# Kernel tuning notes

Measured on AMD Instinct MI355X. Metric: run time of the kernel, lower is better.

## Reference

```python
import jax, jax.numpy as jnp
import numpy as np
from jax import lax

EPS = 1e-3  # keras BatchNormalization default epsilon

def _bn(x, g, b, m, v):
    # inference-mode batchnorm over channel axis (last)
    return (x - m) * (g * lax.rsqrt(v + EPS)) + b

def _cond_dw(h, Wdw, bdw, rw):
    # h: [B,H,W,M]; Wdw: [E,3,3,M]; bdw: [E,M]; rw: [B,E]
    E, M = Wdw.shape[0], Wdw.shape[-1]
    out = jnp.zeros_like(h)
    for i in range(E):  # small fixed expert count
        k = Wdw[i].reshape(3, 3, 1, M)  # depthwise kernel, groups=M
        y = lax.conv_general_dilated(
            h, k, window_strides=(1, 1), padding='SAME',
            dimension_numbers=('NHWC', 'HWIO', 'NHWC'),
            feature_group_count=M) + bdw[i]
        out = out + y * rw[:, i, None, None, None]
    return out

def setup_inputs() -> dict:
    key = jax.random.key(0)
    ks = jax.random.split(key, 24)
    B, H, W, C = 32, 56, 56, 96
    E, M, F = 4, 384, 96
    d = {}
    d['x'] = jax.random.normal(ks[0], (B, H, W, C), jnp.float32)
    d['Wr'] = jax.random.normal(ks[1], (C, E), jnp.float32) * 0.1
    d['br'] = jax.random.normal(ks[2], (E,), jnp.float32) * 0.1
    d['Wpw'] = jax.random.normal(ks[3], (E, C, M), jnp.float32) * (2.0 / C) ** 0.5
    d['bpw'] = jax.random.normal(ks[4], (E, M), jnp.float32) * 0.01
    d['Wdw'] = jax.random.normal(ks[5], (E, 3, 3, M), jnp.float32) * 0.1
    d['bdw'] = jax.random.normal(ks[6], (E, M), jnp.float32) * 0.01
    d['Wpwl'] = jax.random.normal(ks[7], (E, M, F), jnp.float32) * (2.0 / M) ** 0.5
    d['bpwl'] = jax.random.normal(ks[8], (E, F), jnp.float32) * 0.01
    d['g1'] = jax.random.uniform(ks[9], (M,), jnp.float32, 0.5, 1.5)
    d['b1'] = jax.random.normal(ks[10], (M,), jnp.float32) * 0.1
    d['m1'] = jax.random.normal(ks[11], (M,), jnp.float32) * 0.1
    d['v1'] = jax.random.uniform(ks[12], (M,), jnp.float32, 0.5, 1.5)
    d['g2'] = jax.random.uniform(ks[13], (M,), jnp.float32, 0.5, 1.5)
    d['b2'] = jax.random.normal(ks[14], (M,), jnp.float32) * 0.1
    d['m2'] = jax.random.normal(ks[15], (M,), jnp.float32) * 0.1
    d['v2'] = jax.random.uniform(ks[16], (M,), jnp.float32, 0.5, 1.5)
    d['g3'] = jax.random.uniform(ks[17], (F,), jnp.float32, 0.5, 1.5)
    d['b3'] = jax.random.normal(ks[18], (F,), jnp.float32) * 0.1
    d['m3'] = jax.random.normal(ks[19], (F,), jnp.float32) * 0.1
    d['v3'] = jax.random.uniform(ks[20], (F,), jnp.float32, 0.5, 1.5)
    return d

def reference(x, Wr, br, Wpw, bpw, Wdw, bdw, Wpwl, bpwl,
              g1, b1, m1, v1, g2, b2, m2, v2, g3, b3, m3, v3):
    shortcut = x
    # routing: global avg pool + dense + sigmoid
    pooled = jnp.mean(x, axis=(1, 2))                      # [B,C]
    rw = jax.nn.sigmoid(pooled @ Wr + br)                  # [B,E]
    # cond pointwise expand: combine 1x1 expert kernels per-sample (linear in kernel)
    Wk = jnp.einsum('be,ecm->bcm', rw, Wpw)
    h = jnp.einsum('bhwc,bcm->bhwm', x, Wk) + (rw @ bpw)[:, None, None, :]
    h = jax.nn.relu(_bn(h, g1, b1, m1, v1))
    # cond depthwise 3x3
    h = _cond_dw(h, Wdw, bdw, rw)
    h = jax.nn.relu(_bn(h, g2, b2, m2, v2))
    # cond pointwise project
    Wk2 = jnp.einsum('be,emf->bmf', rw, Wpwl)
    h = jnp.einsum('bhwm,bmf->bhwf', h, Wk2) + (rw @ bpwl)[:, None, None, :]
    h = _bn(h, g3, b3, m3, v3)
    return h + shortcut
```

## Files before the change

### kernel.cpp

```cpp
#include <hip/hip_runtime.h>

#define B_ 32
#define HH 56
#define WW 56
#define C_ 96
#define E_ 4
#define M_ 384
#define F_ 96
#define P_ 3136
#define EPS 1e-3f

typedef __attribute__((ext_vector_type(8))) __bf16 bf16x8;
typedef __attribute__((ext_vector_type(8))) short short8;
typedef __attribute__((ext_vector_type(4))) float f32x4;
typedef __attribute__((ext_vector_type(2))) float f32x2;
typedef __attribute__((ext_vector_type(4))) unsigned short us4;
typedef unsigned short u16;

__device__ __forceinline__ float bf2f(u16 s) {
  union { unsigned u; float f; } c;
  c.u = ((unsigned)s) << 16;
  return c.f;
}
__device__ __forceinline__ u16 f2bf(float f) {
  union { float f; unsigned u; } c;
  c.f = f;
  unsigned u = c.u + 0x7FFFu + ((c.u >> 16) & 1u);
  return (u16)(u >> 16);
}
__device__ __forceinline__ f32x2 bfpair(unsigned u) {
  union { unsigned i; float f; } lo, hi;
  lo.i = u << 16;
  hi.i = u & 0xffff0000u;
  f32x2 r;
  r.x = lo.f;
  r.y = hi.f;
  return r;
}

__global__ __launch_bounds__(256) void k_pool(
    const float* __restrict__ x, float* __restrict__ partial) {
  int chunk = blockIdx.x, b = blockIdx.y;
  int p0 = chunk * 49;
  const float* xb = x + ((size_t)b * P_ + p0) * C_;
  int t = threadIdx.x;
  int c4 = t % 24, s = t / 24;
  __shared__ f32x4 part[10][24];
  if (s < 10) {
    f32x4 sum = {0.f, 0.f, 0.f, 0.f};
    for (int p = s; p < 49; p += 10)
      sum += *(const f32x4*)&xb[(size_t)p * C_ + c4 * 4];
    part[s][c4] = sum;
  }
  __syncthreads();
  if (s == 0) {
    f32x4 acc = part[0][c4];
#pragma unroll
    for (int ss = 1; ss < 10; ++ss) acc += part[ss][c4];
    *(f32x4*)&partial[(((size_t)b * 64 + chunk)) * C_ + c4 * 4] = acc;
  }
}

__global__ __launch_bounds__(128) void k_routing2(
    const float* __restrict__ partial, const float* __restrict__ Wr,
    const float* __restrict__ br, float* __restrict__ rw) {
  int b = blockIdx.x;
  int c = threadIdx.x;
  __shared__ float pooled[C_];
  if (c < C_) {
    float s = 0.f;
    for (int ch = 0; ch < 64; ++ch) s += partial[((size_t)b * 64 + ch) * C_ + c];
    pooled[c] = s * (1.f / (float)P_);
  }
  __syncthreads();
  if (c < E_) {
    float acc = br[c];
    for (int cc = 0; cc < C_; ++cc) acc += pooled[cc] * Wr[cc * E_ + c];
    rw[b * E_ + c] = 1.f / (1.f + expf(-acc));
  }
}

__global__ __launch_bounds__(256) void k_mkall(
    const float* __restrict__ Wpw, const float* __restrict__ bpw,
    const float* __restrict__ Wdw, const float* __restrict__ bdw,
    const float* __restrict__ Wpwl, const float* __restrict__ bpwl,
    const float* __restrict__ rw,
    const float* __restrict__ g1, const float* __restrict__ b1,
    const float* __restrict__ m1, const float* __restrict__ v1,
    const float* __restrict__ g2, const float* __restrict__ b2,
    const float* __restrict__ m2, const float* __restrict__ v2,
    const float* __restrict__ g3, const float* __restrict__ b3,
    const float* __restrict__ m3, const float* __restrict__ v3,
    u16* __restrict__ Wk_t, float* __restrict__ bias1p,
    float* __restrict__ Wdwf_t,
    u16* __restrict__ Wk2_t, float* __restrict__ bias3p) {
  int b = blockIdx.x, seg = blockIdx.y;
  float r0 = rw[b * 4 + 0], r1 = rw[b * 4 + 1], r2 = rw[b * 4 + 2], r3 = rw[b * 4 + 3];
  int t = threadIdx.x;
  if (seg < 6) {
    __shared__ __align__(16) u16 tile[64][104];
    int ml = t & 63;
    int m = seg * 64 + ml, cp = t >> 6;
    float s1 = g1[m] * rsqrtf(v1[m] + EPS);
#pragma unroll
    for (int j = 0; j < 24; ++j) {
      int c = cp + 4 * j;
      float w = r0 * Wpw[(0 * C_ + c) * M_ + m] + r1 * Wpw[(1 * C_ + c) * M_ + m] +
                r2 * Wpw[(2 * C_ + c) * M_ + m] + r3 * Wpw[(3 * C_ + c) * M_ + m];
      tile[ml][c] = f2bf(w * s1);
    }
    __syncthreads();
    u16* dst = Wk_t + ((size_t)b * M_ + seg * 64) * C_;
#pragma unroll
    for (int k = 0; k < 3; ++k) {
      int ch = t + 256 * k;
      int mr = ch / 12, off = (ch % 12) * 8;
      *(short8*)&dst[(size_t)mr * C_ + off] = *(const short8*)&tile[mr][off];
    }
  } else if (seg == 6) {
    for (int m = t; m < M_; m += 256) {
      float s2 = g2[m] * rsqrtf(v2[m] + EPS);
      int oct = m >> 3, q = m & 7;
      float* base = Wdwf_t + ((size_t)b * 48 + oct) * 80;
#pragma unroll
      for (int tap = 0; tap < 9; ++tap) {
        float w = r0 * Wdw[(0 * 9 + tap) * M_ + m] + r1 * Wdw[(1 * 9 + tap) * M_ + m] +
                  r2 * Wdw[(2 * 9 + tap) * M_ + m] + r3 * Wdw[(3 * 9 + tap) * M_ + m];
        base[tap * 8 + q] = w * s2;
      }
      float bias = r0 * bdw[m] + r1 * bdw[M_ + m] + r2 * bdw[2 * M_ + m] + r3 * bdw[3 * M_ + m];
      base[72 + q] = (bias - m2[m]) * s2 + b2[m];
      float s1 = g1[m] * rsqrtf(v1[m] + EPS);
      float bb = r0 * bpw[m] + r1 * bpw[M_ + m] + r2 * bpw[2 * M_ + m] + r3 * bpw[3 * M_ + m];
      bias1p[b * M_ + m] = (bb - m1[m]) * s1 + b1[m];
    }
    if (t < F_) {
      float s3 = g3[t] * rsqrtf(v3[t] + EPS);
      float bb = r0 * bpwl[t] + r1 * bpwl[F_ + t] + r2 * bpwl[2 * F_ + t] + r3 * bpwl[3 * F_ + t];
      bias3p[b * F_ + t] = (bb - m3[t]) * s3 + b3[t];
    }
  } else {
    __shared__ __align__(16) u16 tile2[96][72];
    int m0 = (seg - 7) * 64;
#pragma unroll
    for (int j = 0; j < 24; ++j) {
      int id = t + 256 * j;
      int m = id / 96, f = id % 96;
      float w = r0 * Wpwl[(0 * M_ + m0 + m) * F_ + f] + r1 * Wpwl[(1 * M_ + m0 + m) * F_ + f] +
                r2 * Wpwl[(2 * M_ + m0 + m) * F_ + f] + r3 * Wpwl[(3 * M_ + m0 + m) * F_ + f];
      float s3 = g3[f] * rsqrtf(v3[f] + EPS);
      tile2[f][m] = f2bf(w * s3);
    }
    __syncthreads();
    u16* dst = Wk2_t + (size_t)b * F_ * M_ + m0;
#pragma unroll
    for (int k = 0; k < 3; ++k) {
      int ch = t + 256 * k;
      int f = ch / 8, off = (ch % 8) * 8;
      *(short8*)&dst[(size_t)f * M_ + off] = *(const short8*)&tile2[f][off];
    }
  }
}

__global__ __launch_bounds__(256) void k_expand(
    const float* __restrict__ x, const u16* __restrict__ Wk_t,
    const float* __restrict__ bias1p, u16* __restrict__ h1) {
  __shared__ __align__(16) u16 As[64][104];
  __shared__ __align__(16) u16 Bs[64][104];
  int pt = blockIdx.x, b = blockIdx.y;
  int p0 = pt * 64;
  int t = threadIdx.x;
  const float* A = x + ((size_t)b * P_ + p0) * C_;
#pragma unroll
  for (int j = 0; j < 6; ++j) {
    int ch = t + 256 * j;
    int r = ch / 24, o = (ch % 24) * 4;
    f32x4 v = *(const f32x4*)&A[(size_t)r * C_ + o];
    unsigned lo_, hi_;
    asm("v_cvt_pk_bf16_f32 %0, %1, %2" : "=v"(lo_) : "v"(v.x), "v"(v.y));
    asm("v_cvt_pk_bf16_f32 %0, %1, %2" : "=v"(hi_) : "v"(v.z), "v"(v.w));
    uint2 st = {lo_, hi_};
    *(uint2*)&As[r][o] = st;
  }
  const u16* Bt = Wk_t + (size_t)b * M_ * C_;
  u16* out = h1 + (size_t)b * P_ * M_;
  int lane = t & 63, w = t >> 6;
  int rA = w * 16 + (lane & 15);
  int k0 = (lane >> 4) * 8;
  __syncthreads();
  for (int nt = 0; nt < 6; ++nt) {
    if (nt) __syncthreads();
#pragma unroll
    for (int j = 0; j < 3; ++j) {
      int ch = t + 256 * j;
      int r = ch / 12, o = (ch % 12) * 8;
      *(short8*)&Bs[r][o] = *(const short8*)&Bt[((size_t)(nt * 64 + r)) * C_ + o];
    }
    __syncthreads();
    f32x4 acc[4] = {};
#pragma unroll
    for (int kc = 0; kc < 3; ++kc) {
      bf16x8 a = *(const bf16x8*)&As[rA][kc * 32 + k0];
#pragma unroll
      for (int ct = 0; ct < 4; ++ct) {
        bf16x8 bb = *(const bf16x8*)&Bs[ct * 16 + (lane & 15)][kc * 32 + k0];
        acc[ct] = __builtin_amdgcn_mfma_f32_16x16x32_bf16(a, bb, acc[ct], 0, 0, 0);
      }
    }
    int rowb = p0 + w * 16 + (lane >> 4) * 4;
    int n0 = nt * 64;
#pragma unroll
    for (int ct = 0; ct < 4; ++ct) {
      int m = n0 + ct * 16 + (lane & 15);
      float bias = bias1p[b * M_ + m];
#pragma unroll
      for (int i = 0; i < 4; ++i) {
        float v = fmaxf(acc[ct][i] + bias, 0.f);
        out[(size_t)(rowb + i) * M_ + m] = f2bf(v);
      }
    }
  }
}

struct Row { f32x2 v[3][4]; };
__global__ __launch_bounds__(128) void k_dw(
    const u16* __restrict__ h1, const float* __restrict__ Wdwf_t,
    u16* __restrict__ h2) {
  int b = blockIdx.z;
  int t = blockIdx.x * 128 + threadIdx.x;
  int xw = t / 48, oct = t % 48;
  int y0 = blockIdx.y * 7;
  const float* wo = Wdwf_t + ((size_t)b * 48 + oct) * 80;
  f32x2 w2[40];
#pragma unroll
  for (int i = 0; i < 40; ++i) w2[i] = *(const f32x2*)&wo[i * 2];
  const u16* inp = h1 + (size_t)b * P_ * M_ + oct * 8;
  u16* outp = h2 + (size_t)b * P_ * M_ + oct * 8;

  auto loadr = [&](Row& r, int yy) {
    bool rowok = ((unsigned)yy < 56u);
#pragma unroll
    for (int dx = 0; dx < 3; ++dx) {
      int xx = xw + dx - 1;
      uint4 u = {0u, 0u, 0u, 0u};
      if (rowok && ((unsigned)xx < 56u))
        u = *(const uint4*)&inp[((size_t)yy * 56 + xx) * M_];
      r.v[dx][0] = bfpair(u.x);
      r.v[dx][1] = bfpair(u.y);
      r.v[dx][2] = bfpair(u.z);
      r.v[dx][3] = bfpair(u.w);
    }
  };
  auto comp = [&](int y, const Row& A, const Row& B, const Row& C) {
    f32x2 acc[4];
#pragma unroll
    for (int j = 0; j < 4; ++j) acc[j] = w2[36 + j];
#pragma unroll
    for (int dx = 0; dx < 3; ++dx) {
#pragma unroll
      for (int j = 0; j < 4; ++j) {
        acc[j] += A.v[dx][j] * w2[(0 + dx) * 4 + j];
        acc[j] += B.v[dx][j] * w2[(3 + dx) * 4 + j];
        acc[j] += C.v[dx][j] * w2[(6 + dx) * 4 + j];
      }
    }
    unsigned o[4];
#pragma unroll
    for (int j = 0; j < 4; ++j) {
      float lo = fmaxf(acc[j].x, 0.f), hi = fmaxf(acc[j].y, 0.f);
      asm("v_cvt_pk_bf16_f32 %0, %1, %2" : "=v"(o[j]) : "v"(lo), "v"(hi));
    }
    uint4 st = {o[0], o[1], o[2], o[3]};
    *(uint4*)&outp[((size_t)y * 56 + xw) * M_] = st;
  };

  Row ra, rb, rc, rd;
  loadr(ra, y0 - 1);
  loadr(rb, y0);
  loadr(rc, y0 + 1);
  loadr(rd, y0 + 2);
  comp(y0 + 0, ra, rb, rc);
  loadr(ra, y0 + 3);
  comp(y0 + 1, rb, rc, rd);
  loadr(rb, y0 + 4);
  comp(y0 + 2, rc, rd, ra);
  loadr(rc, y0 + 5);
  comp(y0 + 3, rd, ra, rb);
  loadr(rd, y0 + 6);
  comp(y0 + 4, ra, rb, rc);
  loadr(ra, y0 + 7);
  comp(y0 + 5, rb, rc, rd);
  comp(y0 + 6, rc, rd, ra);
}

__global__ __launch_bounds__(256) void k_proj(
    const u16* __restrict__ h2, const u16* __restrict__ Wk2_t,
    const float* __restrict__ bias3p, const float* __restrict__ xres,
    float* __restrict__ outp) {
  __shared__ __align__(16) u16 As[64][104];
  __shared__ __align__(16) u16 Bs[96][104];
  int b = blockIdx.z, pt = blockIdx.x;
  int p0 = pt * 64;
  int t = threadIdx.x;
  const u16* A = h2 + ((size_t)b * P_ + p0) * M_;
  const u16* Bt = Wk2_t + (size_t)b * F_ * M_;
  int lane = t & 63, w = t >> 6;
  int rA = w * 16 + (lane & 15);
  int k0 = (lane >> 4) * 8;
  f32x4 acc[6] = {};
  for (int kc = 0; kc < 4; ++kc) {
    if (kc) __syncthreads();
#pragma unroll
    for (int j = 0; j < 3; ++j) {
      int ch = t + 256 * j;
      int r = ch / 12, o = (ch % 12) * 8;
      *(short8*)&As[r][o] = *(const short8*)&A[(size_t)r * M_ + kc * 96 + o];
    }
#pragma unroll
    for (int j = 0; j < 5; ++j) {
      int ch = t + 256 * j;
      if (ch < 96 * 12) {
        int r = ch / 12, o = (ch % 12) * 8;
        *(short8*)&Bs[r][o] = *(const short8*)&Bt[(size_t)r * M_ + kc * 96 + o];
      }
    }
    __syncthreads();
#pragma unroll
    for (int ks = 0; ks < 3; ++ks) {
      bf16x8 a = *(const bf16x8*)&As[rA][ks * 32 + k0];
#pragma unroll
      for (int ct = 0; ct < 6; ++ct) {
        bf16x8 bb = *(const bf16x8*)&Bs[ct * 16 + (lane & 15)][ks * 32 + k0];
        acc[ct] = __builtin_amdgcn_mfma_f32_16x16x32_bf16(a, bb, acc[ct], 0, 0, 0);
      }
    }
  }
  const float* xr = xres + (size_t)b * P_ * F_;
  float* op = outp + (size_t)b * P_ * F_;
  int rowb = p0 + w * 16 + (lane >> 4) * 4;
#pragma unroll
  for (int ct = 0; ct < 6; ++ct) {
    int f = ct * 16 + (lane & 15);
    float bias = bias3p[b * F_ + f];
#pragma unroll
    for (int i = 0; i < 4; ++i) {
      size_t idx = (size_t)(rowb + i) * F_ + f;
      op[idx] = acc[ct][i] + bias + xr[idx];
    }
  }
}

extern "C" void kernel_launch(void* const* d_in, const int* in_sizes, int n_in,
                              void* d_out, int out_size, void* d_ws, size_t ws_size,
                              hipStream_t stream) {
  (void)in_sizes; (void)n_in; (void)out_size; (void)ws_size;
  const float* x    = (const float*)d_in[0];
  const float* Wr   = (const float*)d_in[1];
  const float* br   = (const float*)d_in[2];
  const float* Wpw  = (const float*)d_in[3];
  const float* bpw  = (const float*)d_in[4];
  const float* Wdw  = (const float*)d_in[5];
  const float* bdw  = (const float*)d_in[6];
  const float* Wpwl = (const float*)d_in[7];
  const float* bpwl = (const float*)d_in[8];
  const float* g1 = (const float*)d_in[9];
  const float* b1 = (const float*)d_in[10];
  const float* m1 = (const float*)d_in[11];
  const float* v1 = (const float*)d_in[12];
  const float* g2 = (const float*)d_in[13];
  const float* b2 = (const float*)d_in[14];
  const float* m2 = (const float*)d_in[15];
  const float* v2 = (const float*)d_in[16];
  const float* g3 = (const float*)d_in[17];
  const float* b3 = (const float*)d_in[18];
  const float* m3 = (const float*)d_in[19];
  const float* v3 = (const float*)d_in[20];
  float* out = (float*)d_out;

  char* p = (char*)d_ws;
  auto alloc = [&](size_t bytes) {
    char* r = p;
    p += (bytes + 255) & ~(size_t)255;
    return r;
  };
  float* rw      = (float*)alloc((size_t)B_ * E_ * 4);
  float* partial = (float*)alloc((size_t)B_ * 64 * C_ * 4);
  u16*   Wk_t    = (u16*)  alloc((size_t)B_ * M_ * C_ * 2);
  float* bias1p  = (float*)alloc((size_t)B_ * M_ * 4);
  float* Wdwf_t  = (float*)alloc((size_t)B_ * 48 * 10 * 8 * 4);
  u16*   Wk2_t   = (u16*)  alloc((size_t)B_ * F_ * M_ * 2);
  float* bias3p  = (float*)alloc((size_t)B_ * F_ * 4);
  u16*   h1      = (u16*)  alloc((size_t)B_ * P_ * M_ * 2);
  u16*   h2      = (u16*)  alloc((size_t)B_ * P_ * M_ * 2);

  k_pool<<<dim3(64, B_), 256, 0, stream>>>(x, partial);
  k_routing2<<<B_, 128, 0, stream>>>(partial, Wr, br, rw);
  k_mkall<<<dim3(B_, 13), 256, 0, stream>>>(Wpw, bpw, Wdw, bdw, Wpwl, bpwl, rw,
                                            g1, b1, m1, v1, g2, b2, m2, v2,
                                            g3, b3, m3, v3,
                                            Wk_t, bias1p, Wdwf_t, Wk2_t, bias3p);
  k_expand<<<dim3(49, B_), 256, 0, stream>>>(x, Wk_t, bias1p, h1);
  k_dw<<<dim3(21, 8, B_), 128, 0, stream>>>(h1, Wdwf_t, h2);
  k_proj<<<dim3(49, 1, B_), 256, 0, stream>>>(h2, Wk2_t, bias3p, x, out);
}
```

Baseline: 129.1 us.

## Store activations channel-octet-major and tile depthwise conv in shared memory

Measured after the change: 136.6 us. +5.9%, slower.

```diff
diff --git a/kernel.cpp b/kernel.cpp
--- a/kernel.cpp
+++ b/kernel.cpp
@@ -38,18 +38,24 @@
   return r;
 }
 
-__global__ __launch_bounds__(256) void k_pool(
-    const float* __restrict__ x, float* __restrict__ partial) {
+__global__ __launch_bounds__(256) void k_pool_convert(
+    const float* __restrict__ x, float* __restrict__ partial, u16* __restrict__ xbf) {
   int chunk = blockIdx.x, b = blockIdx.y;
   int p0 = chunk * 49;
   const float* xb = x + ((size_t)b * P_ + p0) * C_;
+  u16* xo = xbf + ((size_t)b * P_ + p0) * C_;
   int t = threadIdx.x;
   int c4 = t % 24, s = t / 24;
   __shared__ f32x4 part[10][24];
   if (s < 10) {
     f32x4 sum = {0.f, 0.f, 0.f, 0.f};
-    for (int p = s; p < 49; p += 10)
-      sum += *(const f32x4*)&xb[(size_t)p * C_ + c4 * 4];
+    for (int p = s; p < 49; p += 10) {
+      f32x4 v = *(const f32x4*)&xb[(size_t)p * C_ + c4 * 4];
+      sum += v;
+      us4 o;
+      o.x = f2bf(v.x); o.y = f2bf(v.y); o.z = f2bf(v.z); o.w = f2bf(v.w);
+      *(us4*)&xo[(size_t)p * C_ + c4 * 4] = o;
+    }
     part[s][c4] = sum;
   }
   __syncthreads();
@@ -163,27 +169,22 @@
 }
 
 __global__ __launch_bounds__(256) void k_expand(
-    const float* __restrict__ x, const u16* __restrict__ Wk_t,
-    const float* __restrict__ bias1p, u16* __restrict__ h1) {
+    const u16* __restrict__ xbf, const u16* __restrict__ Wk_t,
+    const float* __restrict__ bias1p, u16* __restrict__ h1b) {
   __shared__ __align__(16) u16 As[64][104];
   __shared__ __align__(16) u16 Bs[64][104];
   int pt = blockIdx.x, b = blockIdx.y;
   int p0 = pt * 64;
   int t = threadIdx.x;
-  const float* A = x + ((size_t)b * P_ + p0) * C_;
-#pragma unroll
-  for (int j = 0; j < 6; ++j) {
+  const u16* A = xbf + ((size_t)b * P_ + p0) * C_;
+#pragma unroll
+  for (int j = 0; j < 3; ++j) {
     int ch = t + 256 * j;
-    int r = ch / 24, o = (ch % 24) * 4;
-    f32x4 v = *(const f32x4*)&A[(size_t)r * C_ + o];
-    unsigned lo_, hi_;
-    asm("v_cvt_pk_bf16_f32 %0, %1, %2" : "=v"(lo_) : "v"(v.x), "v"(v.y));
-    asm("v_cvt_pk_bf16_f32 %0, %1, %2" : "=v"(hi_) : "v"(v.z), "v"(v.w));
-    uint2 st = {lo_, hi_};
-    *(uint2*)&As[r][o] = st;
+    int r = ch / 12, o = (ch % 12) * 8;
+    *(short8*)&As[r][o] = *(const short8*)&A[(size_t)r * C_ + o];
   }
   const u16* Bt = Wk_t + (size_t)b * M_ * C_;
-  u16* out = h1 + (size_t)b * P_ * M_;
+  u16* outb = h1b + (size_t)b * 48 * P_ * 8;
   int lane = t & 63, w = t >> 6;
   int rA = w * 16 + (lane & 15);
   int k0 = (lane >> 4) * 8;
@@ -208,60 +209,58 @@
       }
     }
     int rowb = p0 + w * 16 + (lane >> 4) * 4;
-    int n0 = nt * 64;
 #pragma unroll
     for (int ct = 0; ct < 4; ++ct) {
-      int m = n0 + ct * 16 + (lane & 15);
+      int m = nt * 64 + ct * 16 + (lane & 15);
+      int oct = m >> 3, q = m & 7;
       float bias = bias1p[b * M_ + m];
 #pragma unroll
       for (int i = 0; i < 4; ++i) {
         float v = fmaxf(acc[ct][i] + bias, 0.f);
-        out[(size_t)(rowb + i) * M_ + m] = f2bf(v);
-      }
-    }
-  }
-}
-
-struct Row { f32x2 v[3][4]; };
-__global__ __launch_bounds__(128) void k_dw(
-    const u16* __restrict__ h1, const float* __restrict__ Wdwf_t,
-    u16* __restrict__ h2) {
-  int b = blockIdx.z;
-  int t = blockIdx.x * 128 + threadIdx.x;
-  int xw = t / 48, oct = t % 48;
-  int y0 = blockIdx.y * 7;
-  const float* wo = Wdwf_t + ((size_t)b * 48 + oct) * 80;
+        outb[((size_t)oct * P_ + rowb + i) * 8 + q] = f2bf(v);
+      }
+    }
+  }
+}
+
+__global__ __launch_bounds__(512) void k_dw(
+    const u16* __restrict__ h1b, const float* __restrict__ Wdwf_t,
+    u16* __restrict__ h2b) {
+  int oct = blockIdx.x, b = blockIdx.y;
+  int t = threadIdx.x;
+  __shared__ uint4 tile[58 * 58];
+
+  int wbase = __builtin_amdgcn_readfirstlane((b * 48 + oct) * 80);
+  const float* wo = Wdwf_t + wbase;
   f32x2 w2[40];
 #pragma unroll
   for (int i = 0; i < 40; ++i) w2[i] = *(const f32x2*)&wo[i * 2];
-  const u16* inp = h1 + (size_t)b * P_ * M_ + oct * 8;
-  u16* outp = h2 + (size_t)b * P_ * M_ + oct * 8;
-
-  auto loadr = [&](Row& r, int yy) {
-    bool rowok = ((unsigned)yy < 56u);
-#pragma unroll
-    for (int dx = 0; dx < 3; ++dx) {
-      int xx = xw + dx - 1;
-      uint4 u = {0u, 0u, 0u, 0u};
-      if (rowok && ((unsigned)xx < 56u))
-        u = *(const uint4*)&inp[((size_t)yy * 56 + xx) * M_];
-      r.v[dx][0] = bfpair(u.x);
-      r.v[dx][1] = bfpair(u.y);
-      r.v[dx][2] = bfpair(u.z);
-      r.v[dx][3] = bfpair(u.w);
-    }
-  };
-  auto comp = [&](int y, const Row& A, const Row& B, const Row& C) {
-    f32x2 acc[4];
-#pragma unroll
-    for (int j = 0; j < 4; ++j) acc[j] = w2[36 + j];
-#pragma unroll
-    for (int dx = 0; dx < 3; ++dx) {
-#pragma unroll
-      for (int j = 0; j < 4; ++j) {
-        acc[j] += A.v[dx][j] * w2[(0 + dx) * 4 + j];
-        acc[j] += B.v[dx][j] * w2[(3 + dx) * 4 + j];
-        acc[j] += C.v[dx][j] * w2[(6 + dx) * 4 + j];
+
+  const uint4* in = (const uint4*)(h1b + ((size_t)b * 48 + oct) * P_ * 8);
+  uint4* outb = (uint4*)(h2b + ((size_t)b * 48 + oct) * P_ * 8);
+
+  uint4 z = {0u, 0u, 0u, 0u};
+  if (t < 58) { tile[t] = z; tile[57 * 58 + t] = z; }
+  else if (t < 114) { int s = t - 58; tile[(s + 1) * 58] = z; tile[(s + 1) * 58 + 57] = z; }
+  for (int j = t; j < P_; j += 512) {
+    int yy = j / 56, xx = j % 56;
+    tile[(yy + 1) * 58 + xx + 1] = in[j];
+  }
+  __syncthreads();
+
+  for (int i = t; i < P_; i += 512) {
+    int y = i / 56, x = i % 56;
+    f32x2 acc[4] = {w2[36], w2[37], w2[38], w2[39]};
+#pragma unroll
+    for (int dy = 0; dy < 3; ++dy) {
+#pragma unroll
+      for (int dx = 0; dx < 3; ++dx) {
+        uint4 u = tile[(y + dy) * 58 + (x + dx)];
+        int tap = dy * 3 + dx;
+        acc[0] += bfpair(u.x) * w2[tap * 4 + 0];
+        acc[1] += bfpair(u.y) * w2[tap * 4 + 1];
+        acc[2] += bfpair(u.z) * w2[tap * 4 + 2];
+        acc[3] += bfpair(u.w) * w2[tap * 4 + 3];
       }
     }
     unsigned o[4];
@@ -271,38 +270,20 @@
       asm("v_cvt_pk_bf16_f32 %0, %1, %2" : "=v"(o[j]) : "v"(lo), "v"(hi));
     }
     uint4 st = {o[0], o[1], o[2], o[3]};
-    *(uint4*)&outp[((size_t)y * 56 + xw) * M_] = st;
-  };
-
-  Row ra, rb, rc, rd;
-  loadr(ra, y0 - 1);
-  loadr(rb, y0);
-  loadr(rc, y0 + 1);
-  loadr(rd, y0 + 2);
-  comp(y0 + 0, ra, rb, rc);
-  loadr(ra, y0 + 3);
-  comp(y0 + 1, rb, rc, rd);
-  loadr(rb, y0 + 4);
-  comp(y0 + 2, rc, rd, ra);
-  loadr(rc, y0 + 5);
-  comp(y0 + 3, rd, ra, rb);
-  loadr(rd, y0 + 6);
-  comp(y0 + 4, ra, rb, rc);
-  loadr(ra, y0 + 7);
-  comp(y0 + 5, rb, rc, rd);
-  comp(y0 + 6, rc, rd, ra);
+    outb[i] = st;
+  }
 }
 
 __global__ __launch_bounds__(256) void k_proj(
-    const u16* __restrict__ h2, const u16* __restrict__ Wk2_t,
-    const float* __restrict__ bias3p, const float* __restrict__ xres,
+    const u16* __restrict__ h2b, const u16* __restrict__ Wk2_t,
+    const float* __restrict__ bias3p, const u16* __restrict__ xbf,
     float* __restrict__ outp) {
   __shared__ __align__(16) u16 As[64][104];
   __shared__ __align__(16) u16 Bs[96][104];
-  int b = blockIdx.z, pt = blockIdx.x;
+  int pt = blockIdx.x, b = blockIdx.y;
   int p0 = pt * 64;
   int t = threadIdx.x;
-  const u16* A = h2 + ((size_t)b * P_ + p0) * M_;
+  const u16* h2base = h2b + (size_t)b * 48 * P_ * 8;
   const u16* Bt = Wk2_t + (size_t)b * F_ * M_;
   int lane = t & 63, w = t >> 6;
   int rA = w * 16 + (lane & 15);
@@ -313,8 +294,9 @@
 #pragma unroll
     for (int j = 0; j < 3; ++j) {
       int ch = t + 256 * j;
-      int r = ch / 12, o = (ch % 12) * 8;
-      *(short8*)&As[r][o] = *(const short8*)&A[(size_t)r * M_ + kc * 96 + o];
+      int r = ch / 12, ol = ch % 12;
+      *(short8*)&As[r][ol * 8] =
+          *(const short8*)&h2base[((size_t)(kc * 12 + ol) * P_ + p0 + r) * 8];
     }
 #pragma unroll
     for (int j = 0; j < 5; ++j) {
@@ -335,7 +317,7 @@
       }
     }
   }
-  const float* xr = xres + (size_t)b * P_ * F_;
+  const u16* xr = xbf + (size_t)b * P_ * C_;
   float* op = outp + (size_t)b * P_ * F_;
   int rowb = p0 + w * 16 + (lane >> 4) * 4;
 #pragma unroll
@@ -345,7 +327,7 @@
 #pragma unroll
     for (int i = 0; i < 4; ++i) {
       size_t idx = (size_t)(rowb + i) * F_ + f;
-      op[idx] = acc[ct][i] + bias + xr[idx];
+      op[idx] = acc[ct][i] + bias + bf2f(xr[idx]);
     }
   }
 }
@@ -385,21 +367,22 @@
   };
   float* rw      = (float*)alloc((size_t)B_ * E_ * 4);
   float* partial = (float*)alloc((size_t)B_ * 64 * C_ * 4);
+  u16*   xbf     = (u16*)  alloc((size_t)B_ * P_ * C_ * 2);
   u16*   Wk_t    = (u16*)  alloc((size_t)B_ * M_ * C_ * 2);
   float* bias1p  = (float*)alloc((size_t)B_ * M_ * 4);
-  float* Wdwf_t  = (float*)alloc((size_t)B_ * 48 * 10 * 8 * 4);
+  float* Wdwf_t  = (float*)alloc((size_t)B_ * 48 * 80 * 4);
   u16*   Wk2_t   = (u16*)  alloc((size_t)B_ * F_ * M_ * 2);
   float* bias3p  = (float*)alloc((size_t)B_ * F_ * 4);
-  u16*   h1      = (u16*)  alloc((size_t)B_ * P_ * M_ * 2);
-  u16*   h2      = (u16*)  alloc((size_t)B_ * P_ * M_ * 2);
-
-  k_pool<<<dim3(64, B_), 256, 0, stream>>>(x, partial);
+  u16*   h1b     = (u16*)  alloc((size_t)B_ * P_ * M_ * 2);
+  u16*   h2b     = (u16*)  alloc((size_t)B_ * P_ * M_ * 2);
+
+  k_pool_convert<<<dim3(64, B_), 256, 0, stream>>>(x, partial, xbf);
   k_routing2<<<B_, 128, 0, stream>>>(partial, Wr, br, rw);
   k_mkall<<<dim3(B_, 13), 256, 0, stream>>>(Wpw, bpw, Wdw, bdw, Wpwl, bpwl, rw,
                                             g1, b1, m1, v1, g2, b2, m2, v2,
                                             g3, b3, m3, v3,
                                             Wk_t, bias1p, Wdwf_t, Wk2_t, bias3p);
-  k_expand<<<dim3(49, B_), 256, 0, stream>>>(x, Wk_t, bias1p, h1);
-  k_dw<<<dim3(21, 8, B_), 128, 0, stream>>>(h1, Wdwf_t, h2);
-  k_proj<<<dim3(49, 1, B_), 256, 0, stream>>>(h2, Wk2_t, bias3p, x, out);
-}
+  k_expand<<<dim3(49, B_), 256, 0, stream>>>(xbf, Wk_t, bias1p, h1b);
+  k_dw<<<dim3(48, B_), 512, 0, stream>>>(h1b, Wdwf_t, h2b);
+  k_proj<<<dim3(49, B_), 256, 0, stream>>>(h2b, Wk2_t, bias3p, xbf, out);
+}
```
